# Kernel optimization log

Measured on AMD Instinct MI355X. Metric: run time of the kernel, lower is better.

The kernel has to match this reference:

```python
import jax, jax.numpy as jnp
import numpy as np

B, L, C = 32, 2048, 32
PL, STRIDE = 16, 16
P = L // PL
D, H_ENC, H_DEC, K, NH = 64, 256, 256, 512, 4
BETA, EPS, Q_EPS, CW = 0.25, 1e-5, 1e-5, 0.2


def setup_inputs() -> dict:
    key = jax.random.key(0)
    ks = jax.random.split(key, 16)
    g = lambda k, sh: 0.02 * jax.random.normal(k, sh, dtype=jnp.float32)
    return {
        'x': jax.random.normal(ks[0], (B, L, C), dtype=jnp.float32),
        'revin_w': jnp.ones((C,), jnp.float32), 'revin_b': jnp.zeros((C,), jnp.float32),
        'inp_W': g(ks[1], (PL, D)), 'inp_b': jnp.zeros((D,), jnp.float32),
        'Wq': g(ks[2], (D, D)), 'bq': jnp.zeros((D,), jnp.float32),
        'Wk': g(ks[3], (D, D)), 'bk': jnp.zeros((D,), jnp.float32),
        'Wv': g(ks[4], (D, D)), 'bv': jnp.zeros((D,), jnp.float32),
        'Wo': g(ks[5], (D, D)), 'bo': jnp.zeros((D,), jnp.float32),
        'ln1_g': jnp.ones((D,), jnp.float32), 'ln1_b': jnp.zeros((D,), jnp.float32),
        'ffn_W1': g(ks[6], (D, H_ENC)), 'ffn_b1': jnp.zeros((H_ENC,), jnp.float32),
        'ffn_W2': g(ks[7], (H_ENC, D)), 'ffn_b2': jnp.zeros((D,), jnp.float32),
        'ln2_g': jnp.ones((D,), jnp.float32), 'ln2_b': jnp.zeros((D,), jnp.float32),
        'codebook': jax.random.uniform(ks[8], (K, D), jnp.float32, -1.0 / K, 1.0 / K),
        'dec_W1': g(ks[9], (D, H_DEC)), 'dec_b1': jnp.zeros((H_DEC,), jnp.float32),
        'dec_W2': g(ks[10], (H_DEC, PL)), 'dec_b2': jnp.zeros((PL,), jnp.float32),
        'dec_Wr': g(ks[11], (D, PL)), 'dec_br': jnp.zeros((PL,), jnp.float32),
        'dec_ln_g': jnp.ones((PL,), jnp.float32), 'dec_ln_b': jnp.zeros((PL,), jnp.float32),
    }


def _layernorm(x, g, b):
    m = jnp.mean(x, -1, keepdims=True)
    v = jnp.mean((x - m) ** 2, -1, keepdims=True)
    return (x - m) * jax.lax.rsqrt(v + EPS) * g + b


def reference(x, revin_w, revin_b, inp_W, inp_b, Wq, bq, Wk, bk, Wv, bv, Wo, bo,
              ln1_g, ln1_b, ffn_W1, ffn_b1, ffn_W2, ffn_b2, ln2_g, ln2_b, codebook,
              dec_W1, dec_b1, dec_W2, dec_b2, dec_Wr, dec_br, dec_ln_g, dec_ln_b):
    # --- RevIN norm (stats over time dim) ---
    mean = jnp.mean(x, axis=1, keepdims=True)              # [B,1,C]
    std = jnp.sqrt(jnp.var(x, axis=1, keepdims=True) + EPS)
    xn = (x - mean) / std * revin_w + revin_b
    # --- patchify: [B,C,L] -> [B*C, P, PL] ---
    patches = jnp.transpose(xn, (0, 2, 1)).reshape(B * C, P, PL)
    # --- MHEncoder ---
    h = patches @ inp_W + inp_b                            # [N,P,D]
    dh = D // NH
    q = (h @ Wq + bq).reshape(-1, P, NH, dh)
    k = (h @ Wk + bk).reshape(-1, P, NH, dh)
    v = (h @ Wv + bv).reshape(-1, P, NH, dh)
    scores = jnp.einsum('nqhd,nkhd->nhqk', q, k) / np.sqrt(dh).astype(np.float32)
    attn = jax.nn.softmax(scores, axis=-1)
    a = jnp.einsum('nhqk,nkhd->nqhd', attn, v).reshape(-1, P, D)
    a = a @ Wo + bo
    h = _layernorm(h + a, ln1_g, ln1_b)
    ff = jax.nn.relu(h @ ffn_W1 + ffn_b1) @ ffn_W2 + ffn_b2
    h = _layernorm(h + ff, ln2_g, ln2_b)
    z = h.reshape(B, C, P, D)
    # --- ClusterQuantizer ---
    z2 = jnp.sum(z * z, -1, keepdims=True)                 # [B,V,P,1]
    e2 = jnp.sum(codebook * codebook, -1)                  # [K]
    ze = jnp.einsum('bvpd,kd->bvpk', z, codebook)
    dist = z2 + e2 - 2.0 * ze                              # [B,V,P,K]
    indices = jnp.argmin(dist, axis=-1)                    # [B,V,P] int
    z_q = codebook[indices]
    z_q_st = z + jax.lax.stop_gradient(z_q - z)
    codebook_loss = jnp.mean((z_q - jax.lax.stop_gradient(z)) ** 2)
    commitment_loss = jnp.mean((z - jax.lax.stop_gradient(z_q)) ** 2)
    cluster_loss = codebook_loss + BETA * commitment_loss
    counts = jnp.zeros((K,), jnp.float32).at[indices.ravel()].add(1.0)
    probs = counts / (counts.sum() + EPS)
    perplexity = jnp.exp(-jnp.sum(probs * jnp.log(probs + EPS)))
    # --- FFN decoder ---
    y = jax.nn.relu(z_q_st @ dec_W1 + dec_b1) @ dec_W2 + dec_b2
    y = y + z_q_st @ dec_Wr + dec_br
    recon_patches = _layernorm(y, dec_ln_g, dec_ln_b)      # [B,V,P,PL]
    recon = jnp.transpose(recon_patches.reshape(B, C, L), (0, 2, 1))  # [B,L,C]
    # --- RevIN denorm ---
    r = (recon - revin_b) / (revin_w + EPS * EPS) * std + mean
    rec_loss = jnp.mean((x - r) ** 2)
    loss_total = rec_loss + CW * cluster_loss
    return (loss_total, rec_loss, z_q_st, r, indices, perplexity)
```

## Files before the change

### kernel.cpp

```cpp
#include <hip/hip_runtime.h>
#include <math.h>

#define TPB 256

#define B_  32
#define L_  2048
#define C_  32
#define PL_ 16
#define P_  128
#define D_  64
#define HE_ 256
#define HD_ 256
#define K_  512
#define N_  1024
#define M_  131072

#define EPS_  1e-5f
#define BETA_ 0.25f
#define CW_   0.2f

#define OUT_LOSS 0
#define OUT_REC  1
#define OUT_ZQ   2
#define OUT_R    8388610
#define OUT_IDX  10485762
#define OUT_PERP 10616834

#define WS_MEAN   0
#define WS_STD    1024
#define WS_QT     2048
#define WS_KT     6144
#define WS_VT     10240
#define WS_E2     34816
#define WS_COUNTS 35328
#define WS_CPART  35840
#define WS_H0     36864
#define WS_H1     8425472
#define WS_RPART  WS_H1

__global__ void k_prep(const float* __restrict__ Wq, const float* __restrict__ Wk,
                       const float* __restrict__ Wv,
                       const float* __restrict__ cb, float* __restrict__ ws) {
    int g = blockIdx.x * TPB + threadIdx.x;
    if (g < 4096) { int t = g >> 6, j = g & 63; ws[WS_QT + g] = Wq[j * D_ + t]; }
    else if (g < 8192) { int g2 = g - 4096; int t = g2 >> 6, j = g2 & 63; ws[WS_KT + g2] = Wk[j * D_ + t]; }
    else if (g < 12288) { int g2 = g - 8192; int t = g2 >> 6, j = g2 & 63; ws[WS_VT + g2] = Wv[j * D_ + t]; }
    if (g < K_) {
        float s = 0.f;
        for (int j = 0; j < D_; j++) { float v = cb[g * D_ + j]; s += v * v; }
        ws[WS_E2 + g] = s;
    }
}

__global__ void k_stats(const float* __restrict__ x, float* __restrict__ ws) {
    int bc = blockIdx.x;
    int b = bc >> 5, c = bc & 31;
    const float* xp = x + (size_t)b * L_ * C_ + c;
    float s = 0.f, s2 = 0.f;
    for (int l = threadIdx.x; l < L_; l += TPB) { float v = xp[(size_t)l * C_]; s += v; s2 += v * v; }
    __shared__ float sh[TPB], sh2[TPB];
    sh[threadIdx.x] = s; sh2[threadIdx.x] = s2; __syncthreads();
    for (int o2 = 128; o2 > 0; o2 >>= 1) {
        if (threadIdx.x < o2) { sh[threadIdx.x] += sh[threadIdx.x + o2]; sh2[threadIdx.x] += sh2[threadIdx.x + o2]; }
        __syncthreads();
    }
    if (threadIdx.x == 0) {
        float m = sh[0] / (float)L_;
        float var = sh2[0] / (float)L_ - m * m;
        ws[WS_MEAN + bc] = m;
        ws[WS_STD + bc] = sqrtf(var + EPS_);
    }
}

__global__ __launch_bounds__(TPB) void k_embed(
    const float* __restrict__ x, const float* __restrict__ rw, const float* __restrict__ rb,
    const float* __restrict__ inpW, const float* __restrict__ inpb, float* __restrict__ ws) {
    int idx = blockIdx.x * TPB + threadIdx.x;
    int row = idx >> 6, d = idx & 63;
    int n = row >> 7, p = row & 127;
    int b = n >> 5, c = n & 31;
    float m = ws[WS_MEAN + n], sd = ws[WS_STD + n];
    float w = rw[c], bb = rb[c];
    const float* xp = x + (size_t)b * L_ * C_ + (size_t)p * PL_ * C_ + c;
    float acc = inpb[d];
#pragma unroll
    for (int j = 0; j < PL_; j++) {
        float xv = xp[(size_t)j * C_];
        float xn = (xv - m) / sd * w + bb;
        acc += xn * inpW[j * D_ + d];
    }
    ws[WS_H0 + (size_t)idx] = acc;
}

#define HSS  68
#define HS_  0
#define KH_  8704
#define VH_  10752
#define SMF  12800

__global__ __launch_bounds__(TPB) void k_attn(
    float* __restrict__ ws,
    const float* __restrict__ bq, const float* __restrict__ bk, const float* __restrict__ bv) {
    __shared__ float sm[SMF];
    const int tid = threadIdx.x;
    const int n = blockIdx.x >> 2, hh = blockIdx.x & 3;
    const float* h0 = ws + WS_H0 + (size_t)n * (P_ * D_);
    float* agl = ws + WS_H1 + (size_t)n * (P_ * D_);

    {
        const float4* h04 = (const float4*)h0;
#pragma unroll
        for (int it = 0; it < 8; ++it) {
            int e = tid + it * 256;
            int r = e >> 4, j4 = e & 15;
            *(float4*)(sm + HS_ + r * HSS + j4 * 4) = h04[e];
        }
    }
    __syncthreads();

    const int i = tid >> 1, half = tid & 1;
    const int t_ = tid & 15, ib = tid >> 4;
    const float4* WqT4 = (const float4*)(ws + WS_QT);
    const float4* WkT4 = (const float4*)(ws + WS_KT);
    const float4* WvT4 = (const float4*)(ws + WS_VT);

    {
        float4 wreg[16];
        const float4* kr = WkT4 + (size_t)(hh * 16 + t_) * 16;
#pragma unroll
        for (int j4 = 0; j4 < 16; j4++) wreg[j4] = kr[j4];
        float bb = bk[hh * 16 + t_];
#pragma unroll
        for (int it = 0; it < 8; it++) {
            int i2 = ib + it * 16;
            const float4* hr = (const float4*)(sm + HS_ + i2 * HSS);
            float acc = bb;
#pragma unroll
            for (int j4 = 0; j4 < 16; j4++) {
                float4 h4 = hr[j4], w4 = wreg[j4];
                acc += h4.x * w4.x + h4.y * w4.y + h4.z * w4.z + h4.w * w4.w;
            }
            sm[KH_ + i2 * 16 + t_] = acc;
        }
    }
    {
        float4 wreg[16];
        const float4* vr = WvT4 + (size_t)(hh * 16 + t_) * 16;
#pragma unroll
        for (int j4 = 0; j4 < 16; j4++) wreg[j4] = vr[j4];
        float bb = bv[hh * 16 + t_];
#pragma unroll
        for (int it = 0; it < 8; it++) {
            int i2 = ib + it * 16;
            const float4* hr = (const float4*)(sm + HS_ + i2 * HSS);
            float acc = bb;
#pragma unroll
            for (int j4 = 0; j4 < 16; j4++) {
                float4 h4 = hr[j4], w4 = wreg[j4];
                acc += h4.x * w4.x + h4.y * w4.y + h4.z * w4.z + h4.w * w4.w;
            }
            sm[VH_ + i2 * 16 + t_] = acc;
        }
    }
    float q[8];
    {
        float4 hreg[16];
        const float4* hr = (const float4*)(sm + HS_ + i * HSS);
#pragma unroll
        for (int j4 = 0; j4 < 16; j4++) hreg[j4] = hr[j4];
#pragma unroll
        for (int u = 0; u < 8; u++) {
            const float4* wr = WqT4 + (size_t)(hh * 16 + half * 8 + u) * 16;
            float acc = bq[hh * 16 + half * 8 + u];
#pragma unroll
            for (int j4 = 0; j4 < 16; j4++) {
                float4 w4 = wr[j4];
                acc += hreg[j4].x * w4.x + hreg[j4].y * w4.y + hreg[j4].z * w4.z + hreg[j4].w * w4.w;
            }
            q[u] = acc;
        }
    }
    __syncthreads();
    float mx = -INFINITY, S = 0.f;
    float o[8];
#pragma unroll
    for (int u = 0; u < 8; u++) o[u] = 0.f;
    const float4* kh4 = (const float4*)(sm + KH_);
    const float4* vh4 = (const float4*)(sm + VH_);
    for (int ch = 0; ch < 16; ch++) {
        float s[8];
#pragma unroll
        for (int kk = 0; kk < 8; kk++) {
            int m = ch * 8 + kk;
            float4 a0 = kh4[m * 4 + half * 2], a1 = kh4[m * 4 + half * 2 + 1];
            float sp = q[0] * a0.x + q[1] * a0.y + q[2] * a0.z + q[3] * a0.w
                     + q[4] * a1.x + q[5] * a1.y + q[6] * a1.z + q[7] * a1.w;
            s[kk] = (sp + __shfl_xor(sp, 1)) * 0.25f;
        }
        float cm = fmaxf(fmaxf(fmaxf(s[0], s[1]), fmaxf(s[2], s[3])),
                         fmaxf(fmaxf(s[4], s[5]), fmaxf(s[6], s[7])));
        float nM = fmaxf(mx, cm);
        float sc = __expf(mx - nM);
        S *= sc;
#pragma unroll
        for (int u = 0; u < 8; u++) o[u] *= sc;
#pragma unroll
        for (int kk = 0; kk < 8; kk++) {
            int m = ch * 8 + kk;
            float p = __expf(s[kk] - nM);
            S += p;
            float4 v0 = vh4[m * 4 + half * 2], v1 = vh4[m * 4 + half * 2 + 1];
            o[0] += p * v0.x; o[1] += p * v0.y; o[2] += p * v0.z; o[3] += p * v0.w;
            o[4] += p * v1.x; o[5] += p * v1.y; o[6] += p * v1.z; o[7] += p * v1.w;
        }
        mx = nM;
    }
    float inv = 1.f / S;
    float4 r0, r1;
    r0.x = o[0] * inv; r0.y = o[1] * inv; r0.z = o[2] * inv; r0.w = o[3] * inv;
    r1.x = o[4] * inv; r1.y = o[5] * inv; r1.z = o[6] * inv; r1.w = o[7] * inv;
    float4* ap4 = (float4*)(agl + (size_t)i * D_ + hh * 16 + half * 8);
    ap4[0] = r0; ap4[1] = r1;
}

#define FHS  68

__global__ __launch_bounds__(TPB) void k_wo(
    float* __restrict__ ws, const float* __restrict__ Wo, const float* __restrict__ bo,
    const float* __restrict__ g1, const float* __restrict__ b1) {
    __shared__ float aoT[64][FHS];
    const int tid = threadIdx.x;
    const int row0 = blockIdx.x * 64;
    float* aog = ws + WS_H1 + (size_t)row0 * D_;
    {
        const float4* ao4 = (const float4*)aog;
#pragma unroll
        for (int it = 0; it < 4; ++it) {
            int e = tid + it * 256;
            int r = e >> 4, j4 = e & 15;
            float4 v = ao4[e];
            aoT[j4 * 4 + 0][r] = v.x; aoT[j4 * 4 + 1][r] = v.y;
            aoT[j4 * 4 + 2][r] = v.z; aoT[j4 * 4 + 3][r] = v.w;
        }
    }
    const int ty = tid >> 4, tx = tid & 15;
    float acc[4][4];
    {
        float4 bb = ((const float4*)bo)[tx];
#pragma unroll
        for (int r = 0; r < 4; r++) { acc[r][0] = bb.x; acc[r][1] = bb.y; acc[r][2] = bb.z; acc[r][3] = bb.w; }
    }
    __syncthreads();
    const float4* Wo4 = (const float4*)Wo;
#pragma unroll 4
    for (int j = 0; j < 64; ++j) {
        float4 a = *(const float4*)&aoT[j][ty * 4];
        float4 w = Wo4[j * 16 + tx];
        float ar[4] = {a.x, a.y, a.z, a.w}, wr[4] = {w.x, w.y, w.z, w.w};
#pragma unroll
        for (int r = 0; r < 4; r++)
#pragma unroll
            for (int c = 0; c < 4; c++) acc[r][c] += ar[r] * wr[c];
    }
    const float4* h04 = (const float4*)(ws + WS_H0 + (size_t)row0 * D_);
    float4 gg = ((const float4*)g1)[tx], bbn = ((const float4*)b1)[tx];
    float4* h1p = (float4*)aog;
#pragma unroll
    for (int r = 0; r < 4; r++) {
        float4 res = h04[(ty * 4 + r) * 16 + tx];
        acc[r][0] += res.x; acc[r][1] += res.y; acc[r][2] += res.z; acc[r][3] += res.w;
        float s = acc[r][0] + acc[r][1] + acc[r][2] + acc[r][3];
        s += __shfl_xor(s, 1); s += __shfl_xor(s, 2); s += __shfl_xor(s, 4); s += __shfl_xor(s, 8);
        float mean_ = s * (1.f / 64.f);
        float vv = 0.f;
#pragma unroll
        for (int c = 0; c < 4; c++) { float d_ = acc[r][c] - mean_; vv += d_ * d_; }
        vv += __shfl_xor(vv, 1); vv += __shfl_xor(vv, 2); vv += __shfl_xor(vv, 4); vv += __shfl_xor(vv, 8);
        float rstd = 1.f / sqrtf(vv * (1.f / 64.f) + EPS_);
        float4 z;
        z.x = (acc[r][0] - mean_) * rstd * gg.x + bbn.x;
        z.y = (acc[r][1] - mean_) * rstd * gg.y + bbn.y;
        z.z = (acc[r][2] - mean_) * rstd * gg.z + bbn.z;
        z.w = (acc[r][3] - mean_) * rstd * gg.w + bbn.w;
        h1p[(ty * 4 + r) * 16 + tx] = z;
    }
}

#define FR_  64

__global__ __launch_bounds__(TPB) void k_ffn(
    float* __restrict__ ws, const float* __restrict__ fW1,
    const float* __restrict__ fb1, const float* __restrict__ fW2, const float* __restrict__ fb2,
    const float* __restrict__ g2, const float* __restrict__ b2) {
    __shared__ float hT[64][FHS];
    __shared__ float Hc[64][FHS];
    const int tid = threadIdx.x;
    const int row0 = blockIdx.x * FR_;
    const float* h1g = ws + WS_H1 + (size_t)row0 * D_;

    {
        const float4* h14 = (const float4*)h1g;
#pragma unroll
        for (int it = 0; it < 4; ++it) {
            int e = tid + it * 256;
            int r = e >> 4, j4 = e & 15;
            float4 v = h14[e];
            hT[j4 * 4 + 0][r] = v.x; hT[j4 * 4 + 1][r] = v.y;
            hT[j4 * 4 + 2][r] = v.z; hT[j4 * 4 + 3][r] = v.w;
        }
    }
    const int ty = tid >> 4, tx = tid & 15;
    const float4* W14 = (const float4*)fW1;
    const float4* W24 = (const float4*)fW2;
    float out[4][4];
    {
        float4 bb = ((const float4*)fb2)[tx];
#pragma unroll
        for (int r = 0; r < 4; r++) { out[r][0] = bb.x; out[r][1] = bb.y; out[r][2] = bb.z; out[r][3] = bb.w; }
    }
    __syncthreads();

    for (int tc = 0; tc < 4; ++tc) {
        float acc[4][4];
        {
            float4 bb1 = ((const float4*)fb1)[tc * 16 + tx];
#pragma unroll
            for (int r = 0; r < 4; r++) { acc[r][0] = bb1.x; acc[r][1] = bb1.y; acc[r][2] = bb1.z; acc[r][3] = bb1.w; }
        }
#pragma unroll 4
        for (int j = 0; j < 64; ++j) {
            float4 a = *(const float4*)&hT[j][ty * 4];
            float4 w = W14[j * 64 + tc * 16 + tx];
            float ar[4] = {a.x, a.y, a.z, a.w}, wr[4] = {w.x, w.y, w.z, w.w};
#pragma unroll
            for (int r = 0; r < 4; r++)
#pragma unroll
                for (int c = 0; c < 4; c++) acc[r][c] += ar[r] * wr[c];
        }
        __syncthreads();
#pragma unroll
        for (int r = 0; r < 4; r++)
#pragma unroll
            for (int c = 0; c < 4; c++) Hc[tx * 4 + c][ty * 4 + r] = fmaxf(acc[r][c], 0.f);
        __syncthreads();
#pragma unroll 4
        for (int h = 0; h < 64; ++h) {
            float4 a = *(const float4*)&Hc[h][ty * 4];
            float4 w = W24[(tc * 64 + h) * 16 + tx];
            float ar[4] = {a.x, a.y, a.z, a.w}, wr[4] = {w.x, w.y, w.z, w.w};
#pragma unroll
            for (int r = 0; r < 4; r++)
#pragma unroll
                for (int c = 0; c < 4; c++) out[r][c] += ar[r] * wr[c];
        }
    }
    {
        const float4* h14 = (const float4*)h1g;
        float4 gg = ((const float4*)g2)[tx], bb = ((const float4*)b2)[tx];
        float4* zp = (float4*)(ws + WS_H0 + (size_t)row0 * D_);
#pragma unroll
        for (int r = 0; r < 4; r++) {
            float4 res = h14[(ty * 4 + r) * 16 + tx];
            out[r][0] += res.x; out[r][1] += res.y; out[r][2] += res.z; out[r][3] += res.w;
            float s = out[r][0] + out[r][1] + out[r][2] + out[r][3];
            s += __shfl_xor(s, 1); s += __shfl_xor(s, 2); s += __shfl_xor(s, 4); s += __shfl_xor(s, 8);
            float mean_ = s * (1.f / 64.f);
            float vv = 0.f;
#pragma unroll
            for (int c = 0; c < 4; c++) { float d_ = out[r][c] - mean_; vv += d_ * d_; }
            vv += __shfl_xor(vv, 1); vv += __shfl_xor(vv, 2); vv += __shfl_xor(vv, 4); vv += __shfl_xor(vv, 8);
            float rstd = 1.f / sqrtf(vv * (1.f / 64.f) + EPS_);
            float4 z;
            z.x = (out[r][0] - mean_) * rstd * gg.x + bb.x;
            z.y = (out[r][1] - mean_) * rstd * gg.y + bb.y;
            z.z = (out[r][2] - mean_) * rstd * gg.z + bb.z;
            z.w = (out[r][3] - mean_) * rstd * gg.w + bb.w;
            zp[(ty * 4 + r) * 16 + tx] = z;
        }
    }
}

#define QROWS 128
#define QKT   64
#define ZTS   132
#define CBS   68

__global__ __launch_bounds__(TPB) void k_quant(
    float* __restrict__ ws, const float* __restrict__ cb, float* __restrict__ out) {
    __shared__ float zT[64][ZTS];
    __shared__ float cbT[64][CBS];
    __shared__ float z2s[QROWS];
    __shared__ float e2t[QKT];
    __shared__ int   ridx[QROWS];
    __shared__ float red[TPB];

    const int tid = threadIdx.x;
    const int row0 = blockIdx.x * QROWS;
    const float* zg = ws + WS_H0 + (size_t)row0 * D_;
    const float4* zg4 = (const float4*)zg;
    const float4* cbg4 = (const float4*)cb;

    {
        int j4 = tid >> 4;
#pragma unroll
        for (int it = 0; it < 8; ++it) {
            int r = (tid & 15) + it * 16;
            float4 v = zg4[r * 16 + j4];
            zT[j4 * 4 + 0][r] = v.x; zT[j4 * 4 + 1][r] = v.y;
            zT[j4 * 4 + 2][r] = v.z; zT[j4 * 4 + 3][r] = v.w;
        }
    }
    if (tid < QROWS) {
        const float4* zr = (const float4*)(zg + (size_t)tid * D_);
        float s = 0.f;
#pragma unroll
        for (int j = 0; j < 16; j++) { float4 v = zr[j]; s += v.x * v.x + v.y * v.y + v.z * v.z + v.w * v.w; }
        z2s[tid] = s;
    }

    const int ty = tid >> 4, tx = tid & 15;
    float best[8]; int bidx[8];
#pragma unroll
    for (int u = 0; u < 8; u++) { best[u] = 3.4e38f; bidx[u] = 0; }

    for (int t = 0; t < K_ / QKT; ++t) {
        const int k0 = t * QKT;
        __syncthreads();
        {
            int j4 = tid >> 4;
#pragma unroll
            for (int it = 0; it < 4; ++it) {
                int kk = (tid & 15) + it * 16;
                float4 v = cbg4[(size_t)(k0 + kk) * 16 + j4];
                cbT[j4 * 4 + 0][kk] = v.x; cbT[j4 * 4 + 1][kk] = v.y;
                cbT[j4 * 4 + 2][kk] = v.z; cbT[j4 * 4 + 3][kk] = v.w;
            }
        }
        if (tid < QKT) e2t[tid] = ws[WS_E2 + k0 + tid];
        __syncthreads();

        float acc[8][4];
#pragma unroll
        for (int u = 0; u < 8; u++)
#pragma unroll
            for (int c = 0; c < 4; c++) acc[u][c] = 0.f;

        for (int j = 0; j < 64; ++j) {
            float4 a0 = *(const float4*)&zT[j][ty * 8];
            float4 a1 = *(const float4*)&zT[j][ty * 8 + 4];
            float4 b0 = *(const float4*)&cbT[j][tx * 4];
            float ar[8] = {a0.x, a0.y, a0.z, a0.w, a1.x, a1.y, a1.z, a1.w};
            float br[4] = {b0.x, b0.y, b0.z, b0.w};
#pragma unroll
            for (int u = 0; u < 8; u++)
#pragma unroll
                for (int c = 0; c < 4; c++) acc[u][c] += ar[u] * br[c];
        }

#pragma unroll
        for (int u = 0; u < 8; u++) {
            float z2v = z2s[ty * 8 + u];
#pragma unroll
            for (int c = 0; c < 4; c++) {
                float dist = (z2v + e2t[tx * 4 + c]) - 2.f * acc[u][c];
                int kidx = k0 + tx * 4 + c;
                if (dist < best[u]) { best[u] = dist; bidx[u] = kidx; }
            }
        }
    }

#pragma unroll
    for (int m = 1; m <= 8; m <<= 1) {
#pragma unroll
        for (int u = 0; u < 8; u++) {
            float ob = __shfl_xor(best[u], m, 64);
            int oi = __shfl_xor(bidx[u], m, 64);
            if (ob < best[u] || (ob == best[u] && oi < bidx[u])) { best[u] = ob; bidx[u] = oi; }
        }
    }
    if (tx == 0) {
#pragma unroll
        for (int u = 0; u < 8; u++) ridx[ty * 8 + u] = bidx[u];
    }
    __syncthreads();

    if (tid < QROWS) {
        int bi = ridx[tid];
        out[OUT_IDX + row0 + tid] = (float)bi;
        atomicAdd((unsigned int*)ws + WS_COUNTS + bi, 1u);
    }
    {
        int r = tid >> 1, half = tid & 1;
        int bi = ridx[r];
        const float4* cw = (const float4*)(cb + (size_t)bi * D_ + half * 32);
        const float4* zr4 = (const float4*)(zg + (size_t)r * D_ + half * 32);
        float2* zqo = (float2*)(out + OUT_ZQ + (size_t)(row0 + r) * D_ + half * 32);
        float csum = 0.f;
#pragma unroll
        for (int j4 = 0; j4 < 8; ++j4) {
            float4 w = cw[j4]; float4 zz = zr4[j4];
            float d0 = w.x - zz.x, d1 = w.y - zz.y, d2 = w.z - zz.z, d3 = w.w - zz.w;
            csum += d0 * d0 + d1 * d1 + d2 * d2 + d3 * d3;
            float2 p0; p0.x = w.x; p0.y = w.y; zqo[j4 * 2] = p0;
            float2 p1; p1.x = w.z; p1.y = w.w; zqo[j4 * 2 + 1] = p1;
        }
        red[tid] = csum;
    }
    __syncthreads();
    for (int o2 = 128; o2 > 0; o2 >>= 1) {
        if (tid < o2) red[tid] += red[tid + o2];
        __syncthreads();
    }
    if (tid == 0) ws[WS_CPART + blockIdx.x] = red[0];
}

#define DR_ 64

__global__ __launch_bounds__(TPB) void k_dec(
    float* __restrict__ ws, const float* __restrict__ x, const float* __restrict__ cb,
    const float* __restrict__ dW1, const float* __restrict__ db1,
    const float* __restrict__ dW2, const float* __restrict__ db2,
    const float* __restrict__ dWr, const float* __restrict__ dbr,
    const float* __restrict__ lng, const float* __restrict__ lnb,
    const float* __restrict__ rw, const float* __restrict__ rb,
    float* __restrict__ out) {
    __shared__ float zqT[64][FHS];
    __shared__ float Hc[64][FHS];
    __shared__ int   ridx[DR_];
    __shared__ float red[TPB];
    const int tid = threadIdx.x;
    const int row0 = blockIdx.x * DR_;
    if (tid < DR_) ridx[tid] = (int)out[OUT_IDX + row0 + tid];
    __syncthreads();
    {
        const float4* cb4 = (const float4*)cb;
#pragma unroll
        for (int it = 0; it < 4; ++it) {
            int e = tid + it * 256;
            int r = e >> 4, j4 = e & 15;
            float4 v = cb4[(size_t)ridx[r] * 16 + j4];
            zqT[j4 * 4 + 0][r] = v.x; zqT[j4 * 4 + 1][r] = v.y;
            zqT[j4 * 4 + 2][r] = v.z; zqT[j4 * 4 + 3][r] = v.w;
        }
    }
    const int ty = tid >> 4, tx = tid & 15;
    const float4* dW14 = (const float4*)dW1;
    float out4[4];
    {
        float b0 = db2[tx] + dbr[tx];
#pragma unroll
        for (int r = 0; r < 4; r++) out4[r] = b0;
    }
    __syncthreads();

    for (int tc = 0; tc < 4; ++tc) {
        float acc[4][4];
        {
            float4 bb1 = ((const float4*)db1)[tc * 16 + tx];
#pragma unroll
            for (int r = 0; r < 4; r++) { acc[r][0] = bb1.x; acc[r][1] = bb1.y; acc[r][2] = bb1.z; acc[r][3] = bb1.w; }
        }
#pragma unroll 4
        for (int j = 0; j < 64; ++j) {
            float4 a = *(const float4*)&zqT[j][ty * 4];
            float4 w = dW14[j * 64 + tc * 16 + tx];
            float ar[4] = {a.x, a.y, a.z, a.w}, wr[4] = {w.x, w.y, w.z, w.w};
#pragma unroll
            for (int r = 0; r < 4; r++)
#pragma unroll
                for (int c = 0; c < 4; c++) acc[r][c] += ar[r] * wr[c];
        }
        __syncthreads();
#pragma unroll
        for (int r = 0; r < 4; r++)
#pragma unroll
            for (int c = 0; c < 4; c++) Hc[tx * 4 + c][ty * 4 + r] = fmaxf(acc[r][c], 0.f);
        __syncthreads();
#pragma unroll 8
        for (int h = 0; h < 64; ++h) {
            float4 a = *(const float4*)&Hc[h][ty * 4];
            float w = dW2[(tc * 64 + h) * 16 + tx];
            out4[0] += a.x * w; out4[1] += a.y * w; out4[2] += a.z * w; out4[3] += a.w * w;
        }
    }
#pragma unroll 8
    for (int j = 0; j < 64; ++j) {
        float4 a = *(const float4*)&zqT[j][ty * 4];
        float w = dWr[j * 16 + tx];
        out4[0] += a.x * w; out4[1] += a.y * w; out4[2] += a.z * w; out4[3] += a.w * w;
    }
    const int n = row0 >> 7;
    const int b = n >> 5, c = n & 31;
    const float sd = ws[WS_STD + n], mn = ws[WS_MEAN + n];
    const float inv = 1.f / (rw[c] + EPS_ * EPS_);
    const float rbc = rb[c];
    const float lg = lng[tx], lb = lnb[tx];
    float part = 0.f;
#pragma unroll
    for (int r = 0; r < 4; r++) {
        float v = out4[r];
        float s = v;
        s += __shfl_xor(s, 1); s += __shfl_xor(s, 2); s += __shfl_xor(s, 4); s += __shfl_xor(s, 8);
        float mean_ = s * (1.f / 16.f);
        float d_ = v - mean_;
        float vv = d_ * d_;
        vv += __shfl_xor(vv, 1); vv += __shfl_xor(vv, 2); vv += __shfl_xor(vv, 4); vv += __shfl_xor(vv, 8);
        float rstd = 1.f / sqrtf(vv * (1.f / 16.f) + EPS_);
        float yv = d_ * rstd * lg + lb;
        float rr = (yv - rbc) * inv * sd + mn;
        int row = row0 + ty * 4 + r;
        int p = row & 127;
        size_t xi = (size_t)b * L_ * C_ + (size_t)(p * PL_ + tx) * C_ + c;
        out[OUT_R + xi] = rr;
        float dx = x[xi] - rr; part += dx * dx;
    }
    red[tid] = part;
    __syncthreads();
    for (int o2 = 128; o2 > 0; o2 >>= 1) {
        if (tid < o2) red[tid] += red[tid + o2];
        __syncthreads();
    }
    if (tid == 0) ws[WS_RPART + blockIdx.x] = red[0];
}

__global__ void k_final(float* __restrict__ ws, float* __restrict__ out) {
    __shared__ float sh[TPB];
    int tid = threadIdx.x;
    float cs = 0.f;
    for (int i2 = tid; i2 < 1024; i2 += TPB) cs += ws[WS_CPART + i2];
    sh[tid] = cs; __syncthreads();
    for (int o2 = 128; o2 > 0; o2 >>= 1) { if (tid < o2) sh[tid] += sh[tid + o2]; __syncthreads(); }
    float csum = sh[0]; __syncthreads();
    float rs = 0.f;
    for (int i2 = tid; i2 < 2048; i2 += TPB) rs += ws[WS_RPART + i2];
    sh[tid] = rs; __syncthreads();
    for (int o2 = 128; o2 > 0; o2 >>= 1) { if (tid < o2) sh[tid] += sh[tid + o2]; __syncthreads(); }
    float rsum = sh[0]; __syncthreads();
    const unsigned int* counts = (const unsigned int*)ws + WS_COUNTS;
    float H = 0.f;
    for (int k2 = tid; k2 < K_; k2 += TPB) {
        float p = (float)counts[k2] / (131072.f + EPS_);
        H += p * logf(p + EPS_);
    }
    sh[tid] = H; __syncthreads();
    for (int o2 = 128; o2 > 0; o2 >>= 1) { if (tid < o2) sh[tid] += sh[tid + o2]; __syncthreads(); }
    if (tid == 0) {
        float rec = rsum / 2097152.f;
        float msd = csum / 8388608.f;
        float cl = (1.f + BETA_) * msd;
        out[OUT_LOSS] = rec + CW_ * cl;
        out[OUT_REC] = rec;
        out[OUT_PERP] = expf(-sh[0]);
    }
}

extern "C" void kernel_launch(void* const* d_in, const int* in_sizes, int n_in,
                              void* d_out, int out_size, void* d_ws, size_t ws_size,
                              hipStream_t stream) {
    const float* x    = (const float*)d_in[0];
    const float* rw   = (const float*)d_in[1];
    const float* rb   = (const float*)d_in[2];
    const float* inpW = (const float*)d_in[3];
    const float* inpb = (const float*)d_in[4];
    const float* Wq   = (const float*)d_in[5];
    const float* bq   = (const float*)d_in[6];
    const float* Wk   = (const float*)d_in[7];
    const float* bk   = (const float*)d_in[8];
    const float* Wv   = (const float*)d_in[9];
    const float* bv   = (const float*)d_in[10];
    const float* Wo   = (const float*)d_in[11];
    const float* bo   = (const float*)d_in[12];
    const float* g1   = (const float*)d_in[13];
    const float* b1   = (const float*)d_in[14];
    const float* fW1  = (const float*)d_in[15];
    const float* fb1  = (const float*)d_in[16];
    const float* fW2  = (const float*)d_in[17];
    const float* fb2  = (const float*)d_in[18];
    const float* g2   = (const float*)d_in[19];
    const float* b2   = (const float*)d_in[20];
    const float* cb   = (const float*)d_in[21];
    const float* dW1  = (const float*)d_in[22];
    const float* db1  = (const float*)d_in[23];
    const float* dW2  = (const float*)d_in[24];
    const float* db2  = (const float*)d_in[25];
    const float* dWr  = (const float*)d_in[26];
    const float* dbr  = (const float*)d_in[27];
    const float* lng  = (const float*)d_in[28];
    const float* lnb  = (const float*)d_in[29];
    float* ws  = (float*)d_ws;
    float* out = (float*)d_out;

    hipMemsetAsync((char*)d_ws + (size_t)WS_COUNTS * 4, 0, 512 * 4, stream);
    k_prep<<<48, TPB, 0, stream>>>(Wq, Wk, Wv, cb, ws);
    k_stats<<<N_, TPB, 0, stream>>>(x, ws);
    k_embed<<<(M_ * D_) / TPB, TPB, 0, stream>>>(x, rw, rb, inpW, inpb, ws);
    k_attn<<<N_ * 4, TPB, 0, stream>>>(ws, bq, bk, bv);
    k_wo<<<M_ / 64, TPB, 0, stream>>>(ws, Wo, bo, g1, b1);
    k_ffn<<<M_ / FR_, TPB, 0, stream>>>(ws, fW1, fb1, fW2, fb2, g2, b2);
    k_quant<<<M_ / QROWS, TPB, 0, stream>>>(ws, cb, out);
    k_dec<<<M_ / DR_, TPB, 0, stream>>>(ws, x, cb, dW1, db1, dW2, db2, dWr, dbr, lng, lnb, rw, rb, out);
    k_final<<<1, TPB, 0, stream>>>(ws, out);
}
```

Measured before the change: 740.8 us.

## Split attention keys across thread pairs and read hidden rows directly from global

The attention kernel no longer stages the hidden tile in shared memory. The K/V/Q projections read h0 rows straight from global memory, which cuts shared memory from about 50KB to 16KB per block and should allow more resident blocks. Each thread pair now splits the key sequence (even/odd keys) instead of splitting the head dimension, so the per-score shuffle is gone. The two partial softmax states are merged with a log-sum-exp combine at the end. In exchange there are more global loads for h0, which is reread by many threads and relies on cache, and more registers per thread for the 16-wide accumulators.

```diff
diff --git a/kernel.cpp b/kernel.cpp
--- a/kernel.cpp
+++ b/kernel.cpp
@@ -92,11 +92,9 @@
     ws[WS_H0 + (size_t)idx] = acc;
 }
 
-#define HSS  68
-#define HS_  0
-#define KH_  8704
-#define VH_  10752
-#define SMF  12800
+#define KH_  0
+#define VH_  2048
+#define SMF  4096
 
 __global__ __launch_bounds__(TPB) void k_attn(
     float* __restrict__ ws,
@@ -107,18 +105,6 @@
     const float* h0 = ws + WS_H0 + (size_t)n * (P_ * D_);
     float* agl = ws + WS_H1 + (size_t)n * (P_ * D_);
 
-    {
-        const float4* h04 = (const float4*)h0;
-#pragma unroll
-        for (int it = 0; it < 8; ++it) {
-            int e = tid + it * 256;
-            int r = e >> 4, j4 = e & 15;
-            *(float4*)(sm + HS_ + r * HSS + j4 * 4) = h04[e];
-        }
-    }
-    __syncthreads();
-
-    const int i = tid >> 1, half = tid & 1;
     const int t_ = tid & 15, ib = tid >> 4;
     const float4* WqT4 = (const float4*)(ws + WS_QT);
     const float4* WkT4 = (const float4*)(ws + WS_KT);
@@ -133,7 +119,7 @@
 #pragma unroll
         for (int it = 0; it < 8; it++) {
             int i2 = ib + it * 16;
-            const float4* hr = (const float4*)(sm + HS_ + i2 * HSS);
+            const float4* hr = (const float4*)(h0 + (size_t)i2 * D_);
             float acc = bb;
 #pragma unroll
             for (int j4 = 0; j4 < 16; j4++) {
@@ -152,7 +138,7 @@
 #pragma unroll
         for (int it = 0; it < 8; it++) {
             int i2 = ib + it * 16;
-            const float4* hr = (const float4*)(sm + HS_ + i2 * HSS);
+            const float4* hr = (const float4*)(h0 + (size_t)i2 * D_);
             float acc = bb;
 #pragma unroll
             for (int j4 = 0; j4 < 16; j4++) {
@@ -162,12 +148,14 @@
             sm[VH_ + i2 * 16 + t_] = acc;
         }
     }
-    float q[8];
+    const int i = tid >> 1, half = tid & 1;
+    float q0[8], q1[8];
     {
         float4 hreg[16];
-        const float4* hr = (const float4*)(sm + HS_ + i * HSS);
+        const float4* hr = (const float4*)(h0 + (size_t)i * D_);
 #pragma unroll
         for (int j4 = 0; j4 < 16; j4++) hreg[j4] = hr[j4];
+        float qh[8];
 #pragma unroll
         for (int u = 0; u < 8; u++) {
             const float4* wr = WqT4 + (size_t)(hh * 16 + half * 8 + u) * 16;
@@ -177,25 +165,33 @@
                 float4 w4 = wr[j4];
                 acc += hreg[j4].x * w4.x + hreg[j4].y * w4.y + hreg[j4].z * w4.z + hreg[j4].w * w4.w;
             }
-            q[u] = acc;
+            qh[u] = acc;
+        }
+#pragma unroll
+        for (int u = 0; u < 8; u++) {
+            float oth = __shfl_xor(qh[u], 1);
+            q0[u] = half ? oth : qh[u];
+            q1[u] = half ? qh[u] : oth;
         }
     }
     __syncthreads();
     float mx = -INFINITY, S = 0.f;
-    float o[8];
-#pragma unroll
-    for (int u = 0; u < 8; u++) o[u] = 0.f;
+    float o[16];
+#pragma unroll
+    for (int u = 0; u < 16; u++) o[u] = 0.f;
     const float4* kh4 = (const float4*)(sm + KH_);
     const float4* vh4 = (const float4*)(sm + VH_);
-    for (int ch = 0; ch < 16; ch++) {
+    for (int ch = 0; ch < 8; ch++) {
         float s[8];
 #pragma unroll
         for (int kk = 0; kk < 8; kk++) {
-            int m = ch * 8 + kk;
-            float4 a0 = kh4[m * 4 + half * 2], a1 = kh4[m * 4 + half * 2 + 1];
-            float sp = q[0] * a0.x + q[1] * a0.y + q[2] * a0.z + q[3] * a0.w
-                     + q[4] * a1.x + q[5] * a1.y + q[6] * a1.z + q[7] * a1.w;
-            s[kk] = (sp + __shfl_xor(sp, 1)) * 0.25f;
+            int m = (ch * 8 + kk) * 2 + half;
+            float4 a0 = kh4[m * 4 + 0], a1 = kh4[m * 4 + 1], a2 = kh4[m * 4 + 2], a3 = kh4[m * 4 + 3];
+            float sp = q0[0] * a0.x + q0[1] * a0.y + q0[2] * a0.z + q0[3] * a0.w
+                     + q0[4] * a1.x + q0[5] * a1.y + q0[6] * a1.z + q0[7] * a1.w
+                     + q1[0] * a2.x + q1[1] * a2.y + q1[2] * a2.z + q1[3] * a2.w
+                     + q1[4] * a3.x + q1[5] * a3.y + q1[6] * a3.z + q1[7] * a3.w;
+            s[kk] = sp * 0.25f;
         }
         float cm = fmaxf(fmaxf(fmaxf(s[0], s[1]), fmaxf(s[2], s[3])),
                          fmaxf(fmaxf(s[4], s[5]), fmaxf(s[6], s[7])));
@@ -203,24 +199,42 @@
         float sc = __expf(mx - nM);
         S *= sc;
 #pragma unroll
-        for (int u = 0; u < 8; u++) o[u] *= sc;
+        for (int u = 0; u < 16; u++) o[u] *= sc;
 #pragma unroll
         for (int kk = 0; kk < 8; kk++) {
-            int m = ch * 8 + kk;
+            int m = (ch * 8 + kk) * 2 + half;
             float p = __expf(s[kk] - nM);
             S += p;
-            float4 v0 = vh4[m * 4 + half * 2], v1 = vh4[m * 4 + half * 2 + 1];
+            float4 v0 = vh4[m * 4 + 0], v1 = vh4[m * 4 + 1], v2 = vh4[m * 4 + 2], v3 = vh4[m * 4 + 3];
             o[0] += p * v0.x; o[1] += p * v0.y; o[2] += p * v0.z; o[3] += p * v0.w;
             o[4] += p * v1.x; o[5] += p * v1.y; o[6] += p * v1.z; o[7] += p * v1.w;
+            o[8] += p * v2.x; o[9] += p * v2.y; o[10] += p * v2.z; o[11] += p * v2.w;
+            o[12] += p * v3.x; o[13] += p * v3.y; o[14] += p * v3.z; o[15] += p * v3.w;
         }
         mx = nM;
     }
-    float inv = 1.f / S;
-    float4 r0, r1;
-    r0.x = o[0] * inv; r0.y = o[1] * inv; r0.z = o[2] * inv; r0.w = o[3] * inv;
-    r1.x = o[4] * inv; r1.y = o[5] * inv; r1.z = o[6] * inv; r1.w = o[7] * inv;
-    float4* ap4 = (float4*)(agl + (size_t)i * D_ + hh * 16 + half * 8);
-    ap4[0] = r0; ap4[1] = r1;
+    {
+        float mo = __shfl_xor(mx, 1), So = __shfl_xor(S, 1);
+        float nM = fmaxf(mx, mo);
+        float sa = __expf(mx - nM), sb = __expf(mo - nM);
+        float Sc = S * sa + So * sb;
+        float inv = 1.f / Sc;
+        float oo[16];
+#pragma unroll
+        for (int u = 0; u < 16; u++) oo[u] = __shfl_xor(o[u], 1);
+        float wv[8];
+#pragma unroll
+        for (int u = 0; u < 8; u++) {
+            float lo = (o[u] * sa + oo[u] * sb) * inv;
+            float hi = (o[8 + u] * sa + oo[8 + u] * sb) * inv;
+            wv[u] = half ? hi : lo;
+        }
+        float4 r0, r1;
+        r0.x = wv[0]; r0.y = wv[1]; r0.z = wv[2]; r0.w = wv[3];
+        r1.x = wv[4]; r1.y = wv[5]; r1.z = wv[6]; r1.w = wv[7];
+        float4* ap4 = (float4*)(agl + (size_t)i * D_ + hh * 16 + half * 8);
+        ap4[0] = r0; ap4[1] = r1;
+    }
 }
 
 #define FHS  68
```

After: 1.047 ms. 1.41x slower.
